# Performance work log

Measured on AMD Instinct MI355X. Metric: run time of the kernel, lower is better.

Reference implementation:

```python
import jax, jax.numpy as jnp
import numpy as np

NEG_SLOPE = 0.2  # PyG GATConv default negative_slope


def gat_layer(x, src, dst, W, att_src, att_dst, bias, heads, out_ch, n_nodes):
    """PyG-style GATConv (concat=True, add_self_loops already applied via src/dst).
    x: [N, F_in], W: [F_in, heads*out_ch], att_*: [heads, out_ch], bias: [heads*out_ch].
    Returns [N, heads*out_ch]."""
    xh = (x @ W).reshape(n_nodes, heads, out_ch)            # [N,H,C]
    a_src = jnp.einsum('nhc,hc->nh', xh, att_src)           # [N,H]
    a_dst = jnp.einsum('nhc,hc->nh', xh, att_dst)           # [N,H]
    e = a_src[src] + a_dst[dst]                             # [E,H]
    e = jax.nn.leaky_relu(e, NEG_SLOPE)
    # softmax over edges sharing the same destination node
    emax = jax.ops.segment_max(e, dst, num_segments=n_nodes)    # [N,H]
    expe = jnp.exp(e - emax[dst])                           # [E,H]
    denom = jax.ops.segment_sum(expe, dst, num_segments=n_nodes)
    coef = expe / (denom[dst] + 1e-16)                      # [E,H]
    # weighted scatter-aggregate of source features
    msg = xh[src] * coef[:, :, None]                        # [E,H,C]
    out = jax.ops.segment_sum(msg, dst, num_segments=n_nodes)  # [N,H,C]
    return out.reshape(n_nodes, heads * out_ch) + bias


def setup_inputs() -> dict:
    key = jax.random.key(0)
    ks = jax.random.split(key, 10)
    N, E = 50000, 800000
    IN, HID, OUT, H = 4, 60, 96, 8
    x = jax.random.normal(ks[0], (N, IN), dtype=jnp.float32)
    edge_index = jax.random.randint(ks[1], (2, E), 0, N, dtype=jnp.int64)
    s = 0.1
    W1 = jax.random.normal(ks[2], (IN, H * HID), dtype=jnp.float32) * s
    att_src1 = jax.random.normal(ks[3], (H, HID), dtype=jnp.float32) * s
    att_dst1 = jax.random.normal(ks[4], (H, HID), dtype=jnp.float32) * s
    b1 = jnp.zeros((H * HID,), dtype=jnp.float32)
    W2 = jax.random.normal(ks[5], (H * HID, OUT), dtype=jnp.float32) * s
    att_src2 = jax.random.normal(ks[6], (1, OUT), dtype=jnp.float32) * s
    att_dst2 = jax.random.normal(ks[7], (1, OUT), dtype=jnp.float32) * s
    b2 = jnp.zeros((OUT,), dtype=jnp.float32)
    return {"x": x, "edge_index": edge_index,
            "W1": W1, "att_src1": att_src1, "att_dst1": att_dst1, "b1": b1,
            "W2": W2, "att_src2": att_src2, "att_dst2": att_dst2, "b2": b2}


def reference(x, edge_index, W1, att_src1, att_dst1, b1, W2, att_src2, att_dst2, b2):
    N = x.shape[0]
    # add self-loops (PyG GATConv default add_self_loops=True)
    loop = jnp.arange(N, dtype=edge_index.dtype)
    src = jnp.concatenate([edge_index[0], loop])
    dst = jnp.concatenate([edge_index[1], loop])
    # dropout layers are identity in eval mode
    h = gat_layer(x, src, dst, W1, att_src1, att_dst1, b1, heads=8, out_ch=60, n_nodes=N)
    h = jax.nn.elu(h)
    out = gat_layer(h, src, dst, W2, att_src2, att_dst2, b2, heads=1, out_ch=96, n_nodes=N)
    return out
```

## Files before the change

kernel.cpp:

```cpp
#include <hip/hip_runtime.h>
#include <hip/hip_bf16.h>
#include <hip/hip_fp16.h>
#include <cstdint>
#include <cstddef>


typedef _Float16 half8 __attribute__((ext_vector_type(8)));
typedef float floatx4 __attribute__((ext_vector_type(4)));

constexpr int BSH = 7;
constexpr int MAXBUK = 512;

__global__ void prep_kernel(const float* __restrict__ W1,
                            const float* __restrict__ as1, const float* __restrict__ ad1,
                            const float* __restrict__ W2,
                            const float* __restrict__ as2, const float* __restrict__ ad2,
                            float* __restrict__ wa1, float4* __restrict__ w1t,
                            float2* __restrict__ wa2t)
{
    int t = threadIdx.x;
    if (t < 480) {
        float accs = 0.f, accd = 0.f;
        #pragma unroll 4
        for (int c = 0; c < 96; ++c) {
            float w = W2[t * 96 + c];
            accs += w * as2[c];
            accd += w * ad2[c];
        }
        wa2t[t] = make_float2(accs, accd);
        w1t[t]  = make_float4(W1[t], W1[480 + t], W1[960 + t], W1[1440 + t]);
    }
    if (t < 32) {
        int k = t >> 3, h = t & 7;
        float accs = 0.f, accd = 0.f;
        for (int c = 0; c < 60; ++c) {
            float w = W1[k * 480 + h * 60 + c];
            accs += w * as1[h * 60 + c];
            accd += w * ad1[h * 60 + c];
        }
        wa1[k * 8 + h]      = accs;
        wa1[32 + k * 8 + h] = accd;
    }
}

__global__ void w2t_kernel(const float* __restrict__ W2, __half* __restrict__ w2t)
{
    int idx = blockIdx.x * 256 + threadIdx.x;
    if (idx >= 96 * 480) return;
    int n = idx / 480, k = idx - n * 480;
    w2t[idx] = __float2half(W2[k * 96 + n]);
}

__global__ void a1_kernel(const float* __restrict__ x, const float* __restrict__ wa1,
                          float* __restrict__ a_s1, float* __restrict__ a_d1, int N)
{
    int n = blockIdx.x * blockDim.x + threadIdx.x;
    if (n >= N) return;
    float4 xv = *(const float4*)(x + (size_t)n * 4);
    #pragma unroll
    for (int h = 0; h < 8; ++h) {
        float as = xv.x * wa1[h] + xv.y * wa1[8 + h] + xv.z * wa1[16 + h] + xv.w * wa1[24 + h];
        float ad = xv.x * wa1[32 + h] + xv.y * wa1[40 + h] + xv.z * wa1[48 + h] + xv.w * wa1[56 + h];
        a_s1[n * 8 + h] = as;
        a_d1[n * 8 + h] = ad;
    }
}

__global__ __launch_bounds__(256) void bucket_hist(const int* __restrict__ ei, int E, int N,
                                                   int* __restrict__ bcnt)
{
    __shared__ int lcnt[MAXBUK];
    int t = threadIdx.x;
    int nbuk = (N + 127) >> BSH;
    for (int b = t; b < nbuk; b += 256) lcnt[b] = 0;
    __syncthreads();
    #pragma unroll
    for (int u = 0; u < 8; ++u) {
        int e = blockIdx.x * 2048 + u * 256 + t;
        if (e < E + N) {
            int d = (e < E) ? ei[E + e] : (e - E);
            atomicAdd(&lcnt[d >> BSH], 1);
        }
    }
    __syncthreads();
    for (int b = t; b < nbuk; b += 256)
        if (lcnt[b]) atomicAdd(&bcnt[b], lcnt[b]);
}

__global__ __launch_bounds__(512) void bucket_scan(const int* __restrict__ bcnt, int nbuk,
                                                   int* __restrict__ boff,
                                                   int* __restrict__ bcursor,
                                                   int* __restrict__ row_ptr, int N)
{
    __shared__ int wsum[8];
    int t = threadIdx.x, lane = t & 63, wid = t >> 6;
    int v = (t < nbuk) ? bcnt[t] : 0;
    int x = v;
    #pragma unroll
    for (int off = 1; off < 64; off <<= 1) {
        int y = __shfl_up(x, off, 64);
        if (lane >= off) x += y;
    }
    if (lane == 63) wsum[wid] = x;
    __syncthreads();
    if (wid == 0) {
        int wv = (lane < 8) ? wsum[lane] : 0;
        #pragma unroll
        for (int off = 1; off < 8; off <<= 1) {
            int y = __shfl_up(wv, off, 64);
            if (lane >= off) wv += y;
        }
        if (lane < 8) wsum[lane] = wv;
    }
    __syncthreads();
    int excl = (wid ? wsum[wid - 1] : 0) + x - v;
    if (t < nbuk) { boff[t] = excl; bcursor[t] = excl; }
    if (t == nbuk - 1) { boff[nbuk] = excl + v; row_ptr[N] = excl + v; }
}

__global__ __launch_bounds__(256) void multisplit(const int* __restrict__ ei, int E, int N,
                                                  int* __restrict__ bcursor,
                                                  int2* __restrict__ ebuf)
{
    __shared__ int lcnt[MAXBUK];
    __shared__ int lbase[MAXBUK];
    int t = threadIdx.x;
    int nbuk = (N + 127) >> BSH;
    for (int b = t; b < nbuk; b += 256) lcnt[b] = 0;
    __syncthreads();
    constexpr int U = 16;
    int ss[U], dd[U], rk[U];
    bool ok[U];
    #pragma unroll
    for (int u = 0; u < U; ++u) {
        int e = blockIdx.x * (256 * U) + u * 256 + t;
        ok[u] = e < E + N;
        if (ok[u]) {
            if (e < E) { ss[u] = ei[e]; dd[u] = ei[E + e]; } else { ss[u] = dd[u] = e - E; }
            rk[u] = atomicAdd(&lcnt[dd[u] >> BSH], 1);
        }
    }
    __syncthreads();
    for (int b = t; b < nbuk; b += 256)
        lbase[b] = lcnt[b] ? atomicAdd(&bcursor[b], lcnt[b]) : 0;
    __syncthreads();
    #pragma unroll
    for (int u = 0; u < U; ++u)
        if (ok[u]) ebuf[(size_t)lbase[dd[u] >> BSH] + rk[u]] = make_int2(ss[u], dd[u]);
}

__global__ __launch_bounds__(256) void csrfill2(const int2* __restrict__ ebuf,
                                                const int* __restrict__ boff,
                                                int* __restrict__ row_ptr,
                                                int* __restrict__ csr, int N)
{
    int b = blockIdx.x;
    int node0 = b << BSH;
    int nnode = N - node0;  if (nnode > 128) nnode = 128;
    int beg = boff[b], end = boff[b + 1];
    __shared__ int hcnt[128], hcur[128];
    __shared__ int wends[4];
    int t = threadIdx.x;
    if (t < 128) hcnt[t] = 0;
    __syncthreads();
    for (int i = beg + t; i < end; i += 256)
        atomicAdd(&hcnt[ebuf[i].y - node0], 1);
    __syncthreads();
    int lane = t & 63, wid = t >> 6;
    int v = (t < 128) ? hcnt[t] : 0;
    int x = v;
    #pragma unroll
    for (int off = 1; off < 64; off <<= 1) {
        int y = __shfl_up(x, off, 64);
        if (lane >= off) x += y;
    }
    if (lane == 63) wends[wid] = x;
    __syncthreads();
    int excl = x - v + ((wid == 1) ? wends[0] : 0);
    if (t < 128) {
        hcur[t] = excl;
        if (t < nnode) row_ptr[node0 + t] = beg + excl;
    }
    __syncthreads();
    for (int i = beg + t; i < end; i += 256) {
        int2 e = ebuf[i];
        int p = atomicAdd(&hcur[e.y - node0], 1);
        csr[(size_t)beg + p] = e.x;
    }
}

__global__ __launch_bounds__(256) void gat1_agg(
    const int* __restrict__ row_ptr, const int* __restrict__ csr,
    const float* __restrict__ x,
    const float* __restrict__ a_s1, const float* __restrict__ a_d1,
    float* __restrict__ agg, float* __restrict__ ssum, int N)
{
    int gid = blockIdx.x * blockDim.x + threadIdx.x;
    int node = gid >> 6;
    if (node >= N) return;
    int lane = threadIdx.x & 63;
    int half = lane >> 5;
    int sl   = lane & 31;
    int h = sl >> 2, c = sl & 3;
    float adh = a_d1[(size_t)node * 8 + h];

    float aggv = 0.f, sv = 0.f;
    int beg = row_ptr[node], end = row_ptr[node + 1];
    constexpr int U = 4;
    for (int base = beg; base < end; base += 2 * U) {
        int   idx[U];
        float msk[U];
        #pragma unroll
        for (int u = 0; u < U; ++u) {
            int t = base + 2 * u + half;
            msk[u] = (t < end) ? 1.f : 0.f;
            idx[u] = csr[t < end ? t : (end - 1)];
        }
        float xv[U], av[U];
        #pragma unroll
        for (int u = 0; u < U; ++u) xv[u] = x[(size_t)idx[u] * 4 + c];
        #pragma unroll
        for (int u = 0; u < U; ++u) av[u] = a_s1[(size_t)idx[u] * 8 + h];
        #pragma unroll
        for (int u = 0; u < U; ++u) {
            float ev = av[u] + adh;
            ev = ev > 0.f ? ev : 0.2f * ev;
            float p = __expf(ev) * msk[u];
            sv   += p;
            aggv += p * xv[u];
        }
    }
    aggv += __shfl_xor(aggv, 32);
    sv   += __shfl_xor(sv, 32);
    if (lane < 32) {
        agg[(size_t)node * 32 + lane] = aggv;
        if (c == 0) ssum[(size_t)node * 8 + h] = sv;
    }
}

__global__ __launch_bounds__(256) void h_kernel(
    const float* __restrict__ agg, const float* __restrict__ ssum,
    const float4* __restrict__ w1t, const float* __restrict__ b1,
    const float2* __restrict__ wa2t,
    __half* __restrict__ h2buf, float* __restrict__ a2s, float* __restrict__ a2d, int N)
{
    __shared__ float4 w1s[480];
    __shared__ float2 wa2s[480];
    __shared__ float  b1s[480];
    int t = threadIdx.x;
    for (int i = t; i < 480; i += 256) {
        w1s[i]  = w1t[i];
        wa2s[i] = wa2t[i];
        b1s[i]  = b1[i];
    }
    __syncthreads();

    int node = blockIdx.x * 4 + (t >> 6);
    if (node >= N) return;
    int lane = t & 63;
    bool act = lane < 60;

    float psrc = 0.f, pdst = 0.f;
    #pragma unroll
    for (int h = 0; h < 8; ++h) {
        float4 ag  = *(const float4*)(agg + (size_t)node * 32 + h * 4);
        float  inv = 1.f / (ssum[(size_t)node * 8 + h] + 1e-16f);
        if (act) {
            int col = h * 60 + lane;
            float4 w  = w1s[col];
            float raw = ag.x * w.x + ag.y * w.y + ag.z * w.z + ag.w * w.w;
            float v   = raw * inv + b1s[col];
            float o   = v > 0.f ? v : (__expf(v) - 1.f);
            h2buf[(size_t)node * 480 + col] = __float2half(o);
            float2 wz = wa2s[col];
            psrc += o * wz.x;
            pdst += o * wz.y;
        }
    }
    #pragma unroll
    for (int off = 32; off; off >>= 1) {
        psrc += __shfl_xor(psrc, off);
        pdst += __shfl_xor(pdst, off);
    }
    if (lane == 0) { a2s[node] = psrc; a2d[node] = pdst; }
}

__global__ __launch_bounds__(256) void gemm2_mfma(
    const __half* __restrict__ h2, const __half* __restrict__ w2t,
    __half* __restrict__ xh2h, int N)
{
    int wave = threadIdx.x >> 6;
    int lane = threadIdx.x & 63;
    int m0 = blockIdx.x * 64 + wave * 16;
    int ra   = lane & 15;
    int kgrp = lane >> 4;
    int m = m0 + ra;  if (m > N - 1) m = N - 1;

    floatx4 acc[6];
    #pragma unroll
    for (int n = 0; n < 6; ++n) acc[n] = (floatx4){0.f, 0.f, 0.f, 0.f};

    const _Float16* arow = (const _Float16*)(h2 + (size_t)m * 480);
    const _Float16* wt   = (const _Float16*)w2t;
    for (int k0 = 0; k0 < 480; k0 += 32) {
        half8 af = *(const half8*)(arow + k0 + kgrp * 8);
        #pragma unroll
        for (int n = 0; n < 6; ++n) {
            half8 bf = *(const half8*)(wt + (size_t)(n * 16 + ra) * 480 + k0 + kgrp * 8);
            acc[n] = __builtin_amdgcn_mfma_f32_16x16x32_f16(af, bf, acc[n], 0, 0, 0);
        }
    }
    #pragma unroll
    for (int n = 0; n < 6; ++n) {
        int c = n * 16 + ra;
        #pragma unroll
        for (int j = 0; j < 4; ++j) {
            int r = m0 + kgrp * 4 + j;
            if (r < N) xh2h[(size_t)r * 96 + c] = __float2half(acc[n][j]);
        }
    }
}

__global__ __launch_bounds__(256) void gat2_fused(
    const int* __restrict__ row_ptr, const int* __restrict__ csr,
    const float* __restrict__ a_s2, const float* __restrict__ a_d2,
    const __half* __restrict__ xh2h, const float* __restrict__ b2,
    float* __restrict__ out, int N)
{
    int gid = blockIdx.x * blockDim.x + threadIdx.x;
    int node = gid >> 6;
    if (node >= N) return;
    int lane = threadIdx.x & 63;
    bool act = lane < 48;
    float adv = a_d2[node];
    float s = 0.f, ax = 0.f, ay = 0.f;
    int beg = __builtin_amdgcn_readfirstlane(row_ptr[node]);
    int end = __builtin_amdgcn_readfirstlane(row_ptr[node + 1]);
    constexpr int U = 8;
    for (int e0 = beg; e0 < end; e0 += U) {
        int   srcs[U];
        float asv[U];
        #pragma unroll
        for (int u = 0; u < U; ++u) {
            int t = e0 + u;  if (t > end - 1) t = end - 1;
            srcs[u] = __builtin_amdgcn_readfirstlane(csr[t]);
            asv[u]  = a_s2[srcs[u]];
        }
        __half2 gv[U];
        if (act) {
            #pragma unroll
            for (int u = 0; u < U; ++u)
                gv[u] = ((const __half2*)(xh2h + (size_t)srcs[u] * 96))[lane];
        }
        #pragma unroll
        for (int u = 0; u < U; ++u) {
            float ev = asv[u] + adv;
            ev = fmaxf(ev, 0.2f * ev);
            float p = (e0 + u < end) ? __expf(ev) : 0.f;
            s += p;
            if (act) {
                float2 fg = __half22float2(gv[u]);
                ax += p * fg.x;
                ay += p * fg.y;
            }
        }
    }
    float inv = 1.f / (s + 1e-16f);
    if (act) {
        out[(size_t)node * 96 + 2 * lane]     = ax * inv + b2[2 * lane];
        out[(size_t)node * 96 + 2 * lane + 1] = ay * inv + b2[2 * lane + 1];
    }
}

extern "C" void kernel_launch(void* const* d_in, const int* in_sizes, int n_in,
                              void* d_out, int out_size, void* d_ws, size_t ws_size,
                              hipStream_t stream)
{
    const float* x   = (const float*)d_in[0];
    const int*   ei  = (const int*)  d_in[1];
    const float* W1  = (const float*)d_in[2];
    const float* as1 = (const float*)d_in[3];
    const float* ad1 = (const float*)d_in[4];
    const float* b1  = (const float*)d_in[5];
    const float* W2  = (const float*)d_in[6];
    const float* as2 = (const float*)d_in[7];
    const float* ad2 = (const float*)d_in[8];
    const float* b2  = (const float*)d_in[9];
    float* out = (float*)d_out;

    int N  = in_sizes[0] / 4;
    int E  = in_sizes[1] / 2;
    int EP = E + N;
    int NBUK = (N + 127) >> BSH;
    int NBK_H = (EP + 2047) / 2048;
    int NBK_M = (EP + 4095) / 4096;

    float* f = (float*)d_ws;
    float* a_s1  = f;  f += (size_t)N * 8;
    float* a_d1  = f;  f += (size_t)N * 8;
    float* agg   = f;  f += (size_t)N * 32;
    float* ssum  = f;  f += (size_t)N * 8;
    float* a_s2  = f;  f += N;
    float* a_d2  = f;  f += N;
    float* wa1   = f;  f += 64;
    float4* w1t  = (float4*)f;  f += 480 * 4;
    float2* wa2t = (float2*)f;  f += 480 * 2;
    __half* h2buf = (__half*)f;
    __half* hp   = h2buf + (size_t)N * 480;
    __half* xh2h = hp;   hp += (size_t)N * 96;
    __half* w2t  = hp;   hp += 96 * 480;
    int2* ebuf   = (int2*)hp;
    int* ip      = (int*)(ebuf + EP);
    int* row_ptr = ip;  ip += N + 1;
    int* bcnt    = ip;  ip += MAXBUK;
    int* boff    = ip;  ip += MAXBUK + 1;
    int* bcursor = ip;  ip += MAXBUK;
    int* csr     = ip;  ip += EP;

    size_t needed = (size_t)((char*)ip - (char*)d_ws);
    if (needed > ws_size) return;

    hipMemsetAsync(bcnt, 0, MAXBUK * sizeof(int), stream);
    prep_kernel<<<1, 512, 0, stream>>>(W1, as1, ad1, W2, as2, ad2, wa1, w1t, wa2t);
    w2t_kernel<<<(96 * 480 + 255) / 256, 256, 0, stream>>>(W2, w2t);
    a1_kernel<<<(N + 255) / 256, 256, 0, stream>>>(x, wa1, a_s1, a_d1, N);
    bucket_hist<<<NBK_H, 256, 0, stream>>>(ei, E, N, bcnt);
    bucket_scan<<<1, 512, 0, stream>>>(bcnt, NBUK, boff, bcursor, row_ptr, N);
    multisplit<<<NBK_M, 256, 0, stream>>>(ei, E, N, bcursor, ebuf);
    csrfill2<<<NBUK, 256, 0, stream>>>(ebuf, boff, row_ptr, csr, N);
    gat1_agg<<<(N * 64 + 255) / 256, 256, 0, stream>>>(
        row_ptr, csr, x, a_s1, a_d1, agg, ssum, N);
    h_kernel<<<(N + 3) / 4, 256, 0, stream>>>(
        agg, ssum, w1t, b1, wa2t, h2buf, a_s2, a_d2, N);
    gemm2_mfma<<<(N + 63) / 64, 256, 0, stream>>>(h2buf, w2t, xh2h, N);
    gat2_fused<<<(N * 64 + 255) / 256, 256, 0, stream>>>(
        row_ptr, csr, a_s2, a_d2, xh2h, b2, out, N);
}
```

Before: 197.4 us.

## Merge setup kernels and precompute layer-2 edge weights in separate edge-parallel pass

Fuses four small setup kernels (weight prep, W2 transpose, layer-1 attention scores, bucket histogram) into one launch partitioned by block index, removing launch overhead and serialization. csrfill2 now also writes destination indices, and a new p2_kernel computes exp(leaky_relu) per edge in an edge-parallel pass so gat2_fused only loads precomputed weights, with unroll raised to 16. This moves the dependent gather-exp chain out of the node-per-wave loop, but adds extra EP-sized writes and reads (csrdst, pbuf2) and one more launch.

Result: faster. 191.8 us (-2.8%).

```diff
diff --git a/kernel.cpp b/kernel.cpp
--- a/kernel.cpp
+++ b/kernel.cpp
@@ -11,80 +11,86 @@
 constexpr int BSH = 7;
 constexpr int MAXBUK = 512;
 
-__global__ void prep_kernel(const float* __restrict__ W1,
-                            const float* __restrict__ as1, const float* __restrict__ ad1,
-                            const float* __restrict__ W2,
-                            const float* __restrict__ as2, const float* __restrict__ ad2,
-                            float* __restrict__ wa1, float4* __restrict__ w1t,
-                            float2* __restrict__ wa2t)
-{
+__global__ __launch_bounds__(256) void setup_kernel(
+    const float* __restrict__ W1,
+    const float* __restrict__ as1, const float* __restrict__ ad1,
+    const float* __restrict__ W2,
+    const float* __restrict__ as2, const float* __restrict__ ad2,
+    const float* __restrict__ x, const int* __restrict__ ei,
+    int E, int N,
+    float4* __restrict__ w1t, float2* __restrict__ wa2t,
+    __half* __restrict__ w2t,
+    float* __restrict__ a_s1, float* __restrict__ a_d1,
+    int* __restrict__ bcnt,
+    int NW2T, int NA1)
+{
+    __shared__ int   lcnt[MAXBUK];
+    __shared__ float wa1s[64];
+    int b = blockIdx.x;
     int t = threadIdx.x;
-    if (t < 480) {
-        float accs = 0.f, accd = 0.f;
-        #pragma unroll 4
-        for (int c = 0; c < 96; ++c) {
-            float w = W2[t * 96 + c];
-            accs += w * as2[c];
-            accd += w * ad2[c];
-        }
-        wa2t[t] = make_float2(accs, accd);
-        w1t[t]  = make_float4(W1[t], W1[480 + t], W1[960 + t], W1[1440 + t]);
-    }
-    if (t < 32) {
-        int k = t >> 3, h = t & 7;
-        float accs = 0.f, accd = 0.f;
-        for (int c = 0; c < 60; ++c) {
-            float w = W1[k * 480 + h * 60 + c];
-            accs += w * as1[h * 60 + c];
-            accd += w * ad1[h * 60 + c];
-        }
-        wa1[k * 8 + h]      = accs;
-        wa1[32 + k * 8 + h] = accd;
-    }
-}
-
-__global__ void w2t_kernel(const float* __restrict__ W2, __half* __restrict__ w2t)
-{
-    int idx = blockIdx.x * 256 + threadIdx.x;
-    if (idx >= 96 * 480) return;
-    int n = idx / 480, k = idx - n * 480;
-    w2t[idx] = __float2half(W2[k * 96 + n]);
-}
-
-__global__ void a1_kernel(const float* __restrict__ x, const float* __restrict__ wa1,
-                          float* __restrict__ a_s1, float* __restrict__ a_d1, int N)
-{
-    int n = blockIdx.x * blockDim.x + threadIdx.x;
-    if (n >= N) return;
-    float4 xv = *(const float4*)(x + (size_t)n * 4);
-    #pragma unroll
-    for (int h = 0; h < 8; ++h) {
-        float as = xv.x * wa1[h] + xv.y * wa1[8 + h] + xv.z * wa1[16 + h] + xv.w * wa1[24 + h];
-        float ad = xv.x * wa1[32 + h] + xv.y * wa1[40 + h] + xv.z * wa1[48 + h] + xv.w * wa1[56 + h];
-        a_s1[n * 8 + h] = as;
-        a_d1[n * 8 + h] = ad;
-    }
-}
-
-__global__ __launch_bounds__(256) void bucket_hist(const int* __restrict__ ei, int E, int N,
-                                                   int* __restrict__ bcnt)
-{
-    __shared__ int lcnt[MAXBUK];
-    int t = threadIdx.x;
-    int nbuk = (N + 127) >> BSH;
-    for (int b = t; b < nbuk; b += 256) lcnt[b] = 0;
-    __syncthreads();
-    #pragma unroll
-    for (int u = 0; u < 8; ++u) {
-        int e = blockIdx.x * 2048 + u * 256 + t;
-        if (e < E + N) {
-            int d = (e < E) ? ei[E + e] : (e - E);
-            atomicAdd(&lcnt[d >> BSH], 1);
-        }
-    }
-    __syncthreads();
-    for (int b = t; b < nbuk; b += 256)
-        if (lcnt[b]) atomicAdd(&bcnt[b], lcnt[b]);
+    int A1_0 = 1 + NW2T;
+    int H0   = A1_0 + NA1;
+
+    if (b == 0) {
+        for (int i = t; i < 480; i += 256) {
+            float accs = 0.f, accd = 0.f;
+            #pragma unroll 4
+            for (int c = 0; c < 96; ++c) {
+                float w = W2[i * 96 + c];
+                accs += w * as2[c];
+                accd += w * ad2[c];
+            }
+            wa2t[i] = make_float2(accs, accd);
+            w1t[i]  = make_float4(W1[i], W1[480 + i], W1[960 + i], W1[1440 + i]);
+        }
+    } else if (b < A1_0) {
+        int idx = (b - 1) * 256 + t;
+        if (idx < 96 * 480) {
+            int n = idx / 480, k = idx - n * 480;
+            w2t[idx] = __float2half(W2[k * 96 + n]);
+        }
+    } else if (b < H0) {
+        if (t < 32) {
+            int k = t >> 3, h = t & 7;
+            float accs = 0.f, accd = 0.f;
+            for (int c = 0; c < 60; ++c) {
+                float w = W1[k * 480 + h * 60 + c];
+                accs += w * as1[h * 60 + c];
+                accd += w * ad1[h * 60 + c];
+            }
+            wa1s[k * 8 + h]      = accs;
+            wa1s[32 + k * 8 + h] = accd;
+        }
+        __syncthreads();
+        int n = (b - A1_0) * 256 + t;
+        if (n < N) {
+            float4 xv = *(const float4*)(x + (size_t)n * 4);
+            #pragma unroll
+            for (int h = 0; h < 8; ++h) {
+                float as = xv.x * wa1s[h] + xv.y * wa1s[8 + h]
+                         + xv.z * wa1s[16 + h] + xv.w * wa1s[24 + h];
+                float ad = xv.x * wa1s[32 + h] + xv.y * wa1s[40 + h]
+                         + xv.z * wa1s[48 + h] + xv.w * wa1s[56 + h];
+                a_s1[n * 8 + h] = as;
+                a_d1[n * 8 + h] = ad;
+            }
+        }
+    } else {
+        int nbuk = (N + 127) >> BSH;
+        for (int i = t; i < nbuk; i += 256) lcnt[i] = 0;
+        __syncthreads();
+        #pragma unroll
+        for (int u = 0; u < 8; ++u) {
+            int e = (b - H0) * 2048 + u * 256 + t;
+            if (e < E + N) {
+                int d = (e < E) ? ei[E + e] : (e - E);
+                atomicAdd(&lcnt[d >> BSH], 1);
+            }
+        }
+        __syncthreads();
+        for (int i = t; i < nbuk; i += 256)
+            if (lcnt[i]) atomicAdd(&bcnt[i], lcnt[i]);
+    }
 }
 
 __global__ __launch_bounds__(512) void bucket_scan(const int* __restrict__ bcnt, int nbuk,
@@ -152,7 +158,8 @@
 __global__ __launch_bounds__(256) void csrfill2(const int2* __restrict__ ebuf,
                                                 const int* __restrict__ boff,
                                                 int* __restrict__ row_ptr,
-                                                int* __restrict__ csr, int N)
+                                                int* __restrict__ csr,
+                                                int* __restrict__ csrdst, int N)
 {
     int b = blockIdx.x;
     int node0 = b << BSH;
@@ -185,7 +192,8 @@
     for (int i = beg + t; i < end; i += 256) {
         int2 e = ebuf[i];
         int p = atomicAdd(&hcur[e.y - node0], 1);
-        csr[(size_t)beg + p] = e.x;
+        csr[(size_t)beg + p]    = e.x;
+        csrdst[(size_t)beg + p] = e.y;
     }
 }
 
@@ -285,6 +293,36 @@
     if (lane == 0) { a2s[node] = psrc; a2d[node] = pdst; }
 }
 
+__global__ __launch_bounds__(256) void p2_kernel(
+    const int* __restrict__ csr, const int* __restrict__ csrdst,
+    const float* __restrict__ a_s2, const float* __restrict__ a_d2,
+    float* __restrict__ pbuf2, int EP)
+{
+    int i = (blockIdx.x * 256 + threadIdx.x) * 4;
+    if (i + 3 < EP) {
+        int4 s4 = *(const int4*)(csr + i);
+        int4 d4 = *(const int4*)(csrdst + i);
+        float e0 = a_s2[s4.x] + a_d2[d4.x];
+        float e1 = a_s2[s4.y] + a_d2[d4.y];
+        float e2 = a_s2[s4.z] + a_d2[d4.z];
+        float e3 = a_s2[s4.w] + a_d2[d4.w];
+        float4 o;
+        o.x = __expf(fmaxf(e0, 0.2f * e0));
+        o.y = __expf(fmaxf(e1, 0.2f * e1));
+        o.z = __expf(fmaxf(e2, 0.2f * e2));
+        o.w = __expf(fmaxf(e3, 0.2f * e3));
+        *(float4*)(pbuf2 + i) = o;
+    } else {
+        for (int u = 0; u < 4; ++u) {
+            int e = i + u;
+            if (e < EP) {
+                float ev = a_s2[csr[e]] + a_d2[csrdst[e]];
+                pbuf2[e] = __expf(fmaxf(ev, 0.2f * ev));
+            }
+        }
+    }
+}
+
 __global__ __launch_bounds__(256) void gemm2_mfma(
     const __half* __restrict__ h2, const __half* __restrict__ w2t,
     __half* __restrict__ xh2h, int N)
@@ -323,7 +361,7 @@
 
 __global__ __launch_bounds__(256) void gat2_fused(
     const int* __restrict__ row_ptr, const int* __restrict__ csr,
-    const float* __restrict__ a_s2, const float* __restrict__ a_d2,
+    const float* __restrict__ pbuf2,
     const __half* __restrict__ xh2h, const float* __restrict__ b2,
     float* __restrict__ out, int N)
 {
@@ -332,19 +370,20 @@
     if (node >= N) return;
     int lane = threadIdx.x & 63;
     bool act = lane < 48;
-    float adv = a_d2[node];
     float s = 0.f, ax = 0.f, ay = 0.f;
     int beg = __builtin_amdgcn_readfirstlane(row_ptr[node]);
     int end = __builtin_amdgcn_readfirstlane(row_ptr[node + 1]);
-    constexpr int U = 8;
+    constexpr int U = 16;
     for (int e0 = beg; e0 < end; e0 += U) {
         int   srcs[U];
-        float asv[U];
+        float pv[U];
         #pragma unroll
         for (int u = 0; u < U; ++u) {
             int t = e0 + u;  if (t > end - 1) t = end - 1;
             srcs[u] = __builtin_amdgcn_readfirstlane(csr[t]);
-            asv[u]  = a_s2[srcs[u]];
+            float pr = __uint_as_float(
+                __builtin_amdgcn_readfirstlane(__float_as_uint(pbuf2[t])));
+            pv[u] = (e0 + u < end) ? pr : 0.f;
         }
         __half2 gv[U];
         if (act) {
@@ -354,14 +393,11 @@
         }
         #pragma unroll
         for (int u = 0; u < U; ++u) {
-            float ev = asv[u] + adv;
-            ev = fmaxf(ev, 0.2f * ev);
-            float p = (e0 + u < end) ? __expf(ev) : 0.f;
-            s += p;
+            s += pv[u];
             if (act) {
                 float2 fg = __half22float2(gv[u]);
-                ax += p * fg.x;
-                ay += p * fg.y;
+                ax += pv[u] * fg.x;
+                ay += pv[u] * fg.y;
             }
         }
     }
@@ -391,9 +427,12 @@
     int N  = in_sizes[0] / 4;
     int E  = in_sizes[1] / 2;
     int EP = E + N;
-    int NBUK = (N + 127) >> BSH;
+    int NBUK  = (N + 127) >> BSH;
+    int NW2T  = (96 * 480 + 255) / 256;
+    int NA1   = (N + 255) / 256;
     int NBK_H = (EP + 2047) / 2048;
     int NBK_M = (EP + 4095) / 4096;
+    int NSETUP = 1 + NW2T + NA1 + NBK_H;
 
     float* f = (float*)d_ws;
     float* a_s1  = f;  f += (size_t)N * 8;
@@ -402,7 +441,6 @@
     float* ssum  = f;  f += (size_t)N * 8;
     float* a_s2  = f;  f += N;
     float* a_d2  = f;  f += N;
-    float* wa1   = f;  f += 64;
     float4* w1t  = (float4*)f;  f += 480 * 4;
     float2* wa2t = (float2*)f;  f += 480 * 2;
     __half* h2buf = (__half*)f;
@@ -416,23 +454,26 @@
     int* boff    = ip;  ip += MAXBUK + 1;
     int* bcursor = ip;  ip += MAXBUK;
     int* csr     = ip;  ip += EP;
+    int* csrdst  = ip;  ip += EP;
+    float* pbuf2 = (float*)ip;  ip += EP;
 
     size_t needed = (size_t)((char*)ip - (char*)d_ws);
     if (needed > ws_size) return;
 
     hipMemsetAsync(bcnt, 0, MAXBUK * sizeof(int), stream);
-    prep_kernel<<<1, 512, 0, stream>>>(W1, as1, ad1, W2, as2, ad2, wa1, w1t, wa2t);
-    w2t_kernel<<<(96 * 480 + 255) / 256, 256, 0, stream>>>(W2, w2t);
-    a1_kernel<<<(N + 255) / 256, 256, 0, stream>>>(x, wa1, a_s1, a_d1, N);
-    bucket_hist<<<NBK_H, 256, 0, stream>>>(ei, E, N, bcnt);
+    setup_kernel<<<NSETUP, 256, 0, stream>>>(
+        W1, as1, ad1, W2, as2, ad2, x, ei, E, N,
+        w1t, wa2t, w2t, a_s1, a_d1, bcnt, NW2T, NA1);
     bucket_scan<<<1, 512, 0, stream>>>(bcnt, NBUK, boff, bcursor, row_ptr, N);
     multisplit<<<NBK_M, 256, 0, stream>>>(ei, E, N, bcursor, ebuf);
-    csrfill2<<<NBUK, 256, 0, stream>>>(ebuf, boff, row_ptr, csr, N);
+    csrfill2<<<NBUK, 256, 0, stream>>>(ebuf, boff, row_ptr, csr, csrdst, N);
     gat1_agg<<<(N * 64 + 255) / 256, 256, 0, stream>>>(
         row_ptr, csr, x, a_s1, a_d1, agg, ssum, N);
     h_kernel<<<(N + 3) / 4, 256, 0, stream>>>(
         agg, ssum, w1t, b1, wa2t, h2buf, a_s2, a_d2, N);
+    p2_kernel<<<(EP + 1023) / 1024, 256, 0, stream>>>(
+        csr, csrdst, a_s2, a_d2, pbuf2, EP);
     gemm2_mfma<<<(N + 63) / 64, 256, 0, stream>>>(h2buf, w2t, xh2h, N);
     gat2_fused<<<(N * 64 + 255) / 256, 256, 0, stream>>>(
-        row_ptr, csr, a_s2, a_d2, xh2h, b2, out, N);
-}
+        row_ptr, csr, pbuf2, xh2h, b2, out, N);
+}
```
